# Performance work log

Measured on AMD Instinct MI355X. Metric: run time of the kernel, lower is better.

Reference implementation:

```python
import jax, jax.numpy as jnp
import numpy as np

D_IN = 2048
D_OUT = 2048
NUM_HEADS = 16
NUM_KV_GROUPS = 4
GROUP_SIZE = NUM_HEADS // NUM_KV_GROUPS  # 4
HEAD_DIM = D_OUT // NUM_HEADS            # 128


def setup_inputs() -> dict:
    key = jax.random.key(0)
    ks = jax.random.split(key, 6)
    b, n = 2, 2048
    x = jax.random.normal(ks[0], (b, n, D_IN), dtype=jnp.float32)
    # weights stored as [in, out] so that x @ W matches torch's x @ weight.T
    Wq = jax.random.normal(ks[1], (D_IN, D_OUT), dtype=jnp.float32) * (1.0 / np.sqrt(D_IN))
    Wk = jax.random.normal(ks[2], (D_IN, NUM_KV_GROUPS * HEAD_DIM), dtype=jnp.float32) * (1.0 / np.sqrt(D_IN))
    Wv = jax.random.normal(ks[3], (D_IN, NUM_KV_GROUPS * HEAD_DIM), dtype=jnp.float32) * (1.0 / np.sqrt(D_IN))
    Wo = jax.random.normal(ks[4], (D_OUT, D_OUT), dtype=jnp.float32) * (1.0 / np.sqrt(D_OUT))
    bo = jax.random.normal(ks[5], (D_OUT,), dtype=jnp.float32) * 0.01
    return {"x": x, "Wq": Wq, "Wk": Wk, "Wv": Wv, "Wo": Wo, "bo": bo}


def reference(x, Wq, Wk, Wv, Wo, bo):
    b, n, _ = x.shape
    # projections
    q = (x @ Wq).reshape(b, n, NUM_KV_GROUPS, GROUP_SIZE, HEAD_DIM)  # [b,n,g,s,d]
    k = (x @ Wk).reshape(b, n, NUM_KV_GROUPS, HEAD_DIM)              # [b,n,g,d]
    v = (x @ Wv).reshape(b, n, NUM_KV_GROUPS, HEAD_DIM)
    scale = 1.0 / np.sqrt(HEAD_DIM).astype(np.float32)
    # scores: each group of GROUP_SIZE query heads shares one K/V head
    scores = jnp.einsum('bqgsd,bkgd->bgsqk', q, k) * scale  # [b,g,s,n,n]
    causal = jnp.arange(n)[:, None] < jnp.arange(n)[None, :]  # True above diagonal
    scores = jnp.where(causal, -jnp.inf, scores)
    attn = jax.nn.softmax(scores, axis=-1)
    # dropout omitted for determinism (eval-mode equivalent)
    ctx = jnp.einsum('bgsqk,bkgd->bqgsd', attn, v)  # [b,n,g,s,d]
    ctx = ctx.reshape(b, n, D_OUT)
    return ctx @ Wo + bo
```

## Files before the change

### kernel.cpp

```cpp
#include <hip/hip_runtime.h>
#include <hip/hip_bf16.h>

typedef short bf16x8 __attribute__((ext_vector_type(8)));
typedef float f32x4 __attribute__((ext_vector_type(4)));
typedef float f32x16 __attribute__((ext_vector_type(16)));
typedef unsigned int u32x4 __attribute__((ext_vector_type(4)));

#define MFMA16(a, b, c) __builtin_amdgcn_mfma_f32_16x16x32_bf16((a), (b), (c), 0, 0, 0)
#define MFMA32(a, b, c) __builtin_amdgcn_mfma_f32_32x32x16_bf16((a), (b), (c), 0, 0, 0)

static __device__ __forceinline__ unsigned short f2bf(float f) {
  union { float f; unsigned u; } v;
  v.f = f;
  unsigned r = (v.u + 0x7FFFu + ((v.u >> 16) & 1u)) >> 16;
  return (unsigned short)r;
}

static __device__ __forceinline__ unsigned pk2(float a, float b) {
  unsigned ua = __float_as_uint(a) + 0x8000u;
  unsigned ub = __float_as_uint(b) + 0x8000u;
  return (ua >> 16) | (ub & 0xFFFF0000u);
}

static __device__ __forceinline__ void gload16(const void* g, void* l) {
  __builtin_amdgcn_global_load_lds(
      (const __attribute__((address_space(1))) unsigned int*)g,
      (__attribute__((address_space(3))) unsigned int*)l, 16, 0, 0);
}

__global__ __launch_bounds__(256) void prep_all2(
    const float* __restrict__ x, unsigned short* __restrict__ Xb,
    const float* __restrict__ Wq, const float* __restrict__ Wk,
    const float* __restrict__ Wv, const float* __restrict__ Wo,
    unsigned short* __restrict__ WqT, unsigned short* __restrict__ WkT,
    unsigned short* __restrict__ WvT, unsigned short* __restrict__ WoT) {
  int id = blockIdx.x;
  if (id >= 10240) {
    const int n4 = (4096 * 2048) / 4;
    const int stride = 2048 * 256;
    for (int i = (id - 10240) * 256 + threadIdx.x; i < n4; i += stride) {
      float4 v = reinterpret_cast<const float4*>(x)[i];
      ushort4 o;
      o.x = f2bf(v.x); o.y = f2bf(v.y); o.z = f2bf(v.z); o.w = f2bf(v.w);
      reinterpret_cast<ushort4*>(Xb)[i] = o;
    }
    return;
  }
  __shared__ float tile[32][33];
  const float* src; unsigned short* dst; int R, C, bx, by;
  if (id < 4096)      { src = Wq; dst = WqT; R = 2048; C = 2048; bx = id & 63; by = id >> 6; }
  else if (id < 5120) { id -= 4096; src = Wk; dst = WkT; R = 2048; C = 512; bx = id & 15; by = id >> 4; }
  else if (id < 6144) { id -= 5120; src = Wv; dst = WvT; R = 2048; C = 512; bx = id & 15; by = id >> 4; }
  else                { id -= 6144; src = Wo; dst = WoT; R = 2048; C = 2048; bx = id & 63; by = id >> 6; }
  int tx = threadIdx.x & 31;
  int ty = threadIdx.x >> 5;
  int r0 = by * 32, c0 = bx * 32;
#pragma unroll
  for (int i = 0; i < 32; i += 8)
    tile[ty + i][tx] = src[(size_t)(r0 + ty + i) * C + (c0 + tx)];
  __syncthreads();
#pragma unroll
  for (int i = 0; i < 32; i += 8)
    dst[(size_t)(c0 + ty + i) * R + (r0 + tx)] = f2bf(tile[tx][ty + i]);
}

template <int EPI>
static __device__ __forceinline__ void g8p_core(
    const unsigned short* __restrict__ A, const unsigned short* __restrict__ B,
    unsigned short* __restrict__ Cb, unsigned short* __restrict__ Cb2,
    float* __restrict__ Cf, const float* __restrict__ bias,
    int N, int K, int bid, unsigned short* Al, unsigned short* Bl) {
  const int tid = threadIdx.x;
  const int wave = tid >> 6, lane = tid & 63;
  const int l15 = lane & 15, l4 = lane >> 4;
  const int tilesN = N >> 7;
  const int bm = bid / tilesN, bn = bid % tilesN;
  const int row0 = bm << 8, col0 = bn << 7;
  const int wr = (wave >> 1) << 6;
  const int wc = (wave & 1) << 6;

  const unsigned short* sA[4];
  const unsigned short* sB[2];
#pragma unroll
  for (int i = 0; i < 4; ++i) {
    int q = i * 512 + wave * 64 + lane;
    int r = q >> 3, c = (q & 7) ^ (r & 7);
    sA[i] = A + (size_t)(row0 + r) * K + c * 8;
  }
#pragma unroll
  for (int i = 0; i < 2; ++i) {
    int q = i * 512 + wave * 64 + lane;
    int r = q >> 3, c = (q & 7) ^ (r & 7);
    sB[i] = B + (size_t)(col0 + r) * K + c * 8;
  }

#define STG_H1(t_, bi)                                                      \
  { const size_t ko = (size_t)(t_) * 64;                                    \
    gload16(sA[0] + ko, &Al[(bi)*16384 + (0 * 512 + wave * 64) * 8]);       \
    gload16(sA[1] + ko, &Al[(bi)*16384 + (1 * 512 + wave * 64) * 8]);       \
    gload16(sB[0] + ko, &Bl[(bi)*8192 + (0 * 512 + wave * 64) * 8]); }
#define STG_H2(t_, bi)                                                      \
  { const size_t ko = (size_t)(t_) * 64;                                    \
    gload16(sA[2] + ko, &Al[(bi)*16384 + (2 * 512 + wave * 64) * 8]);       \
    gload16(sA[3] + ko, &Al[(bi)*16384 + (3 * 512 + wave * 64) * 8]);       \
    gload16(sB[1] + ko, &Bl[(bi)*8192 + (1 * 512 + wave * 64) * 8]); }

  const int sw = l15 & 7;
  const int c0 = (l4 ^ sw) << 4;
  const int c1 = ((4 + l4) ^ sw) << 4;
  const int rbA = (wr + l15) << 7;
  const int rbB = (wc + l15) << 7;

  f32x4 acc[4][4] = {};
  const int NT = K >> 6;

  STG_H1(0, 0); STG_H2(0, 0);
  STG_H1(1, 1); STG_H2(1, 1);

  int cur = 0;
  for (int t = 0; t < NT; ++t) {
    int sb = cur + 2; if (sb >= 3) sb -= 3;
    if (t + 1 < NT) { asm volatile("s_waitcnt vmcnt(6)" ::: "memory"); }
    else            { asm volatile("s_waitcnt vmcnt(0)" ::: "memory"); }
    __builtin_amdgcn_s_barrier();
    asm volatile("" ::: "memory");
    const char* Ab = (const char*)&Al[cur * 16384];
    const char* Bb = (const char*)&Bl[cur * 8192];
    bf16x8 b0[4], b1[4], aA[2][2], aB[2][2];
#pragma unroll
    for (int n = 0; n < 4; ++n) {
      b0[n] = *(const bf16x8*)(Bb + rbB + n * 2048 + c0);
      b1[n] = *(const bf16x8*)(Bb + rbB + n * 2048 + c1);
    }
#pragma unroll
    for (int m = 0; m < 2; ++m) {
      aA[m][0] = *(const bf16x8*)(Ab + rbA + m * 2048 + c0);
      aA[m][1] = *(const bf16x8*)(Ab + rbA + m * 2048 + c1);
    }
    if (t + 2 < NT) STG_H1(t + 2, sb);
    asm volatile("" ::: "memory");
    __builtin_amdgcn_s_barrier();
    asm volatile("" ::: "memory");
    __builtin_amdgcn_s_setprio(1);
#pragma unroll
    for (int m = 0; m < 2; ++m)
#pragma unroll
      for (int n = 0; n < 4; ++n) {
        acc[m][n] = MFMA16(aA[m][0], b0[n], acc[m][n]);
        acc[m][n] = MFMA16(aA[m][1], b1[n], acc[m][n]);
      }
    __builtin_amdgcn_s_setprio(0);
#pragma unroll
    for (int m = 0; m < 2; ++m) {
      aB[m][0] = *(const bf16x8*)(Ab + rbA + (m + 2) * 2048 + c0);
      aB[m][1] = *(const bf16x8*)(Ab + rbA + (m + 2) * 2048 + c1);
    }
    if (t + 2 < NT) STG_H2(t + 2, sb);
    asm volatile("" ::: "memory");
    __builtin_amdgcn_s_barrier();
    asm volatile("" ::: "memory");
    __builtin_amdgcn_s_setprio(1);
#pragma unroll
    for (int m = 0; m < 2; ++m)
#pragma unroll
      for (int n = 0; n < 4; ++n) {
        acc[m + 2][n] = MFMA16(aB[m][0], b0[n], acc[m + 2][n]);
        acc[m + 2][n] = MFMA16(aB[m][1], b1[n], acc[m + 2][n]);
      }
    __builtin_amdgcn_s_setprio(0);
    cur += 1; if (cur >= 3) cur = 0;
  }
#undef STG_H1
#undef STG_H2

#pragma unroll
  for (int m = 0; m < 4; ++m) {
#pragma unroll
    for (int n = 0; n < 4; ++n) {
      int row = row0 + wr + m * 16 + l4 * 4;
      int col = col0 + wc + n * 16 + l15;
#pragma unroll
      for (int r = 0; r < 4; ++r) {
        if (EPI == 0) {
          Cb[(size_t)(row + r) * N + col] = f2bf(acc[m][n][r]);
        } else if (EPI == 1) {
          Cf[(size_t)(row + r) * N + col] = acc[m][n][r] + bias[col];
        } else {
          if (col < 2048) Cb[(size_t)(row + r) * 2048 + col] = f2bf(acc[m][n][r]);
          else            Cb2[(size_t)(row + r) * 512 + col - 2048] = f2bf(acc[m][n][r]);
        }
      }
    }
  }
}

__global__ __launch_bounds__(512, 2) void gemm8p_o(
    const unsigned short* __restrict__ A, const unsigned short* __restrict__ B,
    float* __restrict__ Cf, const float* __restrict__ bias, int N, int K) {
  __shared__ unsigned short Al[3 * 256 * 64];
  __shared__ unsigned short Bl[3 * 128 * 64];
  g8p_core<1>(A, B, nullptr, nullptr, Cf, bias, N, K, blockIdx.x, Al, Bl);
}

__global__ __launch_bounds__(512, 2) void gemm_fused3(
    const unsigned short* __restrict__ Xb, const unsigned short* __restrict__ Bqk,
    unsigned short* __restrict__ Qb, unsigned short* __restrict__ Kb,
    const unsigned short* __restrict__ WvT, unsigned short* __restrict__ VTb) {
  __shared__ unsigned short Al[3 * 256 * 64];
  __shared__ unsigned short Bl[3 * 128 * 64];
  if (blockIdx.x < 320)
    g8p_core<2>(Xb, Bqk, Qb, Kb, nullptr, nullptr, 2560, 2048, blockIdx.x, Al, Bl);
  else
    g8p_core<0>(WvT, Xb, VTb, nullptr, nullptr, nullptr, 4096, 2048, blockIdx.x - 320, Al, Bl);
}

__global__ __launch_bounds__(256, 2) void flash_gqa7c(
    const unsigned short* __restrict__ Qb, const unsigned short* __restrict__ Kb,
    const unsigned short* __restrict__ VT, unsigned short* __restrict__ Ctx) {
  __shared__ unsigned short Sm[32768];

  const int tid = threadIdx.x;
  const int wave = tid >> 6, lane = tid & 63;
  const int l31 = lane & 31, hi = lane >> 5;
  const int i = blockIdx.x >> 3;
  const int bg = blockIdx.x & 7;
  const int qt = (i < 32) ? i : (95 - i);
  const int b = bg >> 2, g = bg & 3;
  const int h = (g << 2) | wave;
  const int q0 = qt << 5;
  const int T = (qt >> 1) + 1;

  bf16x8 qf[8];
  {
    const unsigned short* qp =
        Qb + (size_t)(b * 2048 + q0 + l31) * 2048 + h * 128 + hi * 8;
#pragma unroll
    for (int ds = 0; ds < 8; ++ds) qf[ds] = *(const bf16x8*)(qp + ds * 16);
  }

  const int cK = tid & 15, rK = tid >> 4;
  const unsigned short* kS0 = Kb + (size_t)(b * 2048 + rK +  0) * 512 + g * 128 + (cK ^ ((rK +  0) & 7)) * 8;
  const unsigned short* kS1 = Kb + (size_t)(b * 2048 + rK + 16) * 512 + g * 128 + (cK ^ ((rK + 16) & 7)) * 8;
  const unsigned short* kS2 = Kb + (size_t)(b * 2048 + rK + 32) * 512 + g * 128 + (cK ^ ((rK + 32) & 7)) * 8;
  const unsigned short* kS3 = Kb + (size_t)(b * 2048 + rK + 48) * 512 + g * 128 + (cK ^ ((rK + 48) & 7)) * 8;
  const int cV = tid & 7, rV = tid >> 3;
  const unsigned short* vS0 = VT + (size_t)(g * 128 + rV +  0) * 4096 + b * 2048 + (cV ^ ((rV +  0) & 7)) * 8;
  const unsigned short* vS1 = VT + (size_t)(g * 128 + rV + 32) * 4096 + b * 2048 + (cV ^ ((rV + 32) & 7)) * 8;
  const unsigned short* vS2 = VT + (size_t)(g * 128 + rV + 64) * 4096 + b * 2048 + (cV ^ ((rV + 64) & 7)) * 8;
  const unsigned short* vS3 = VT + (size_t)(g * 128 + rV + 96) * 4096 + b * 2048 + (cV ^ ((rV + 96) & 7)) * 8;

#define STAGE7(t_, bi)                                          \
  {                                                             \
    unsigned short* kb_ = Sm + (bi)*8192;                       \
    unsigned short* vb_ = Sm + 16384 + (bi)*8192;               \
    const size_t ko_ = (size_t)(t_) * 64 * 512;                 \
    const size_t vo_ = (size_t)(t_) * 64;                       \
    gload16(kS0 + ko_, kb_ + 0 * 2048 + wave * 512);            \
    gload16(kS1 + ko_, kb_ + 1 * 2048 + wave * 512);            \
    gload16(kS2 + ko_, kb_ + 2 * 2048 + wave * 512);            \
    gload16(kS3 + ko_, kb_ + 3 * 2048 + wave * 512);            \
    gload16(vS0 + vo_, vb_ + 0 * 2048 + wave * 512);            \
    gload16(vS1 + vo_, vb_ + 1 * 2048 + wave * 512);            \
    gload16(vS2 + vo_, vb_ + 2 * 2048 + wave * 512);            \
    gload16(vS3 + vo_, vb_ + 3 * 2048 + wave * 512);            \
  }

  const float s2 = 0.12751744f;
  float m_r = -1e30f, l_r = 0.f;
  f32x16 o0 = {}, o1 = {}, o2 = {}, o3 = {};

  STAGE7(0, 0);
  __syncthreads();

  for (int t = 0; t < T; ++t) {
    const int buf = t & 1;
    if (t + 1 < T) STAGE7(t + 1, buf ^ 1);
    const char* Kl = (const char*)Sm + buf * 16384;
    const char* Vl = (const char*)Sm + 32768 + buf * 16384;
    const int kv = t << 6;
    f32x16 st0 = {}, st1 = {};
    __builtin_amdgcn_s_setprio(1);
#pragma unroll
    for (int ds = 0; ds < 8; ++ds) {
      const int c = ds * 32 + hi * 16;
      const int by0 = (l31 * 256 + c) ^ ((l31 & 7) << 4);
      const int by1 = ((32 + l31) * 256 + c) ^ ((l31 & 7) << 4);
      bf16x8 kf0 = *(const bf16x8*)(Kl + by0);
      bf16x8 kf1 = *(const bf16x8*)(Kl + by1);
      st0 = MFMA32(kf0, qf[ds], st0);
      st1 = MFMA32(kf1, qf[ds], st1);
    }
    __builtin_amdgcn_s_setprio(0);
    const int q_abs = q0 + l31;
    if (kv + 64 > q0) {
#pragma unroll
      for (int rr = 0; rr < 16; ++rr) {
        const int koff = (rr & 3) + 8 * (rr >> 2) + 4 * hi;
        if (kv + koff > q_abs) st0[rr] = -1e30f;
        if (kv + 32 + koff > q_abs) st1[rr] = -1e30f;
      }
    }
    float pm = st0[0];
#pragma unroll
    for (int rr = 1; rr < 16; ++rr) pm = fmaxf(pm, st0[rr]);
#pragma unroll
    for (int rr = 0; rr < 16; ++rr) pm = fmaxf(pm, st1[rr]);
    pm = fmaxf(pm, __shfl_xor(pm, 32));
    if (!__all(pm - m_r <= 90.0f)) {
      const float mn = fmaxf(m_r, pm);
      const float osc = exp2f((m_r - mn) * s2);
      m_r = mn;
      l_r *= osc;
#pragma unroll
      for (int rr = 0; rr < 16; ++rr) {
        o0[rr] *= osc; o1[rr] *= osc; o2[rr] *= osc; o3[rr] *= osc;
      }
    }
    const float cfold = -m_r * s2;
    float ps = 0.f;
#pragma unroll
    for (int rr = 0; rr < 16; ++rr) { st0[rr] = exp2f(fmaf(st0[rr], s2, cfold)); ps += st0[rr]; }
#pragma unroll
    for (int rr = 0; rr < 16; ++rr) { st1[rr] = exp2f(fmaf(st1[rr], s2, cfold)); ps += st1[rr]; }
    ps += __shfl_xor(ps, 32);
    l_r += ps;
    unsigned w0[8], w1[8];
#pragma unroll
    for (int rp = 0; rp < 8; ++rp) {
      w0[rp] = pk2(st0[2 * rp], st0[2 * rp + 1]);
      w1[rp] = pk2(st1[2 * rp], st1[2 * rp + 1]);
    }
    __builtin_amdgcn_s_setprio(1);
#define PV_KS(ks, W)                                                          \
    {                                                                         \
      const int k4 = ((ks) & 1) * 4;                                          \
      unsigned a0 = W[k4], a1 = W[k4 + 1], b0 = W[k4 + 2], b1 = W[k4 + 3];    \
      unsigned q0_ = hi ? a0 : b0, q1_ = hi ? a1 : b1;                        \
      unsigned e0 = (unsigned)__shfl_xor((int)q0_, 32);                       \
      unsigned e1 = (unsigned)__shfl_xor((int)q1_, 32);                       \
      union { u32x4 u; bf16x8 v; } pk;                                        \
      pk.u[0] = hi ? e0 : a0; pk.u[1] = hi ? e1 : a1;                         \
      pk.u[2] = hi ? b0 : e0; pk.u[3] = hi ? b1 : e1;                         \
      const int cb = (ks)*32 + hi * 16;                                       \
      { const int row = l31;      const int by = (row * 128 + cb) ^ ((row & 7) << 4); \
        bf16x8 vf = *(const bf16x8*)(Vl + by); o0 = MFMA32(vf, pk.v, o0); }   \
      { const int row = 32 + l31; const int by = (row * 128 + cb) ^ ((row & 7) << 4); \
        bf16x8 vf = *(const bf16x8*)(Vl + by); o1 = MFMA32(vf, pk.v, o1); }   \
      { const int row = 64 + l31; const int by = (row * 128 + cb) ^ ((row & 7) << 4); \
        bf16x8 vf = *(const bf16x8*)(Vl + by); o2 = MFMA32(vf, pk.v, o2); }   \
      { const int row = 96 + l31; const int by = (row * 128 + cb) ^ ((row & 7) << 4); \
        bf16x8 vf = *(const bf16x8*)(Vl + by); o3 = MFMA32(vf, pk.v, o3); }   \
    }
    PV_KS(0, w0) PV_KS(1, w0) PV_KS(2, w1) PV_KS(3, w1)
#undef PV_KS
    __builtin_amdgcn_s_setprio(0);
    __syncthreads();
  }
#undef STAGE7

  const float inv = 1.f / l_r;
  unsigned short* cp = Ctx + (size_t)(b * 2048 + q0 + l31) * 2048 + h * 128;
#pragma unroll
  for (int a = 0; a < 4; ++a) {
    ushort4 p0, p1, p2, p3;
    p0.x = f2bf(o0[4 * a + 0] * inv); p0.y = f2bf(o0[4 * a + 1] * inv);
    p0.z = f2bf(o0[4 * a + 2] * inv); p0.w = f2bf(o0[4 * a + 3] * inv);
    p1.x = f2bf(o1[4 * a + 0] * inv); p1.y = f2bf(o1[4 * a + 1] * inv);
    p1.z = f2bf(o1[4 * a + 2] * inv); p1.w = f2bf(o1[4 * a + 3] * inv);
    p2.x = f2bf(o2[4 * a + 0] * inv); p2.y = f2bf(o2[4 * a + 1] * inv);
    p2.z = f2bf(o2[4 * a + 2] * inv); p2.w = f2bf(o2[4 * a + 3] * inv);
    p3.x = f2bf(o3[4 * a + 0] * inv); p3.y = f2bf(o3[4 * a + 1] * inv);
    p3.z = f2bf(o3[4 * a + 2] * inv); p3.w = f2bf(o3[4 * a + 3] * inv);
    const int cc = 8 * a + 4 * hi;
    *(ushort4*)(cp + 0 * 32 + cc) = p0;
    *(ushort4*)(cp + 1 * 32 + cc) = p1;
    *(ushort4*)(cp + 2 * 32 + cc) = p2;
    *(ushort4*)(cp + 3 * 32 + cc) = p3;
  }
}

extern "C" void kernel_launch(void* const* d_in, const int* in_sizes, int n_in,
                              void* d_out, int out_size, void* d_ws, size_t ws_size,
                              hipStream_t stream) {
  (void)in_sizes; (void)n_in; (void)out_size; (void)ws_size;
  const float* x  = (const float*)d_in[0];
  const float* Wq = (const float*)d_in[1];
  const float* Wk = (const float*)d_in[2];
  const float* Wv = (const float*)d_in[3];
  const float* Wo = (const float*)d_in[4];
  const float* bo = (const float*)d_in[5];
  float* out = (float*)d_out;

  unsigned short* Xb  = (unsigned short*)d_ws;
  unsigned short* WqT = Xb  + (size_t)4096 * 2048;
  unsigned short* WkT = WqT + (size_t)2048 * 2048;
  unsigned short* WvT = WkT + (size_t)512 * 2048;
  unsigned short* WoT = WvT + (size_t)512 * 2048;
  unsigned short* Qb  = WoT + (size_t)2048 * 2048;
  unsigned short* Kb  = Qb  + (size_t)4096 * 2048;
  unsigned short* VTb = Kb  + (size_t)4096 * 512;
  unsigned short* Ctx = VTb + (size_t)512 * 4096;

  prep_all2<<<12288, 256, 0, stream>>>(x, Xb, Wq, Wk, Wv, Wo, WqT, WkT, WvT, WoT);

  gemm_fused3<<<dim3(384), 512, 0, stream>>>(Xb, WqT, Qb, Kb, WvT, VTb);

  flash_gqa7c<<<dim3(512), 256, 0, stream>>>(Qb, Kb, VTb, Ctx);

  gemm8p_o<<<dim3(256), 512, 0, stream>>>(Ctx, WoT, out, bo, 2048, 2048);
}
```

Measured before the change: 192.8 us.

## Load V fragments directly from global memory and remap GEMM block indices

The flash attention kernel no longer stages V tiles through shared memory. Each lane reads its V^T fragment straight from global memory inside the PV loop, which halves LDS use per block and could allow more resident blocks. The cost is global-load latency sitting directly in the MFMA dependency chain. Separately, the GEMM kernels remap blockIdx so that consecutively launched blocks are spread across XCDs in a strided order, aiming at better L2 locality.

New measurement: 240.8 us. 1.25x slower.

```diff
diff --git a/kernel.cpp b/kernel.cpp
--- a/kernel.cpp
+++ b/kernel.cpp
@@ -199,7 +199,8 @@
     float* __restrict__ Cf, const float* __restrict__ bias, int N, int K) {
   __shared__ unsigned short Al[3 * 256 * 64];
   __shared__ unsigned short Bl[3 * 128 * 64];
-  g8p_core<1>(A, B, nullptr, nullptr, Cf, bias, N, K, blockIdx.x, Al, Bl);
+  int bid = (blockIdx.x & 7) * 32 + (blockIdx.x >> 3);
+  g8p_core<1>(A, B, nullptr, nullptr, Cf, bias, N, K, bid, Al, Bl);
 }
 
 __global__ __launch_bounds__(512, 2) void gemm_fused3(
@@ -208,16 +209,20 @@
     const unsigned short* __restrict__ WvT, unsigned short* __restrict__ VTb) {
   __shared__ unsigned short Al[3 * 256 * 64];
   __shared__ unsigned short Bl[3 * 128 * 64];
-  if (blockIdx.x < 320)
-    g8p_core<2>(Xb, Bqk, Qb, Kb, nullptr, nullptr, 2560, 2048, blockIdx.x, Al, Bl);
-  else
-    g8p_core<0>(WvT, Xb, VTb, nullptr, nullptr, nullptr, 4096, 2048, blockIdx.x - 320, Al, Bl);
-}
-
-__global__ __launch_bounds__(256, 2) void flash_gqa7c(
+  if (blockIdx.x < 320) {
+    int bid = (blockIdx.x & 7) * 40 + (blockIdx.x >> 3);
+    g8p_core<2>(Xb, Bqk, Qb, Kb, nullptr, nullptr, 2560, 2048, bid, Al, Bl);
+  } else {
+    int lb = blockIdx.x - 320;
+    int bid = (lb & 7) * 8 + (lb >> 3);
+    g8p_core<0>(WvT, Xb, VTb, nullptr, nullptr, nullptr, 4096, 2048, bid, Al, Bl);
+  }
+}
+
+__global__ __launch_bounds__(256, 2) void flash_gqa7d(
     const unsigned short* __restrict__ Qb, const unsigned short* __restrict__ Kb,
     const unsigned short* __restrict__ VT, unsigned short* __restrict__ Ctx) {
-  __shared__ unsigned short Sm[32768];
+  __shared__ unsigned short Sm[16384];
 
   const int tid = threadIdx.x;
   const int wave = tid >> 6, lane = tid & 63;
@@ -243,26 +248,20 @@
   const unsigned short* kS1 = Kb + (size_t)(b * 2048 + rK + 16) * 512 + g * 128 + (cK ^ ((rK + 16) & 7)) * 8;
   const unsigned short* kS2 = Kb + (size_t)(b * 2048 + rK + 32) * 512 + g * 128 + (cK ^ ((rK + 32) & 7)) * 8;
   const unsigned short* kS3 = Kb + (size_t)(b * 2048 + rK + 48) * 512 + g * 128 + (cK ^ ((rK + 48) & 7)) * 8;
-  const int cV = tid & 7, rV = tid >> 3;
-  const unsigned short* vS0 = VT + (size_t)(g * 128 + rV +  0) * 4096 + b * 2048 + (cV ^ ((rV +  0) & 7)) * 8;
-  const unsigned short* vS1 = VT + (size_t)(g * 128 + rV + 32) * 4096 + b * 2048 + (cV ^ ((rV + 32) & 7)) * 8;
-  const unsigned short* vS2 = VT + (size_t)(g * 128 + rV + 64) * 4096 + b * 2048 + (cV ^ ((rV + 64) & 7)) * 8;
-  const unsigned short* vS3 = VT + (size_t)(g * 128 + rV + 96) * 4096 + b * 2048 + (cV ^ ((rV + 96) & 7)) * 8;
+
+  const unsigned short* vG0 = VT + (size_t)(g * 128 +  0 + l31) * 4096 + b * 2048 + hi * 8;
+  const unsigned short* vG1 = VT + (size_t)(g * 128 + 32 + l31) * 4096 + b * 2048 + hi * 8;
+  const unsigned short* vG2 = VT + (size_t)(g * 128 + 64 + l31) * 4096 + b * 2048 + hi * 8;
+  const unsigned short* vG3 = VT + (size_t)(g * 128 + 96 + l31) * 4096 + b * 2048 + hi * 8;
 
 #define STAGE7(t_, bi)                                          \
   {                                                             \
     unsigned short* kb_ = Sm + (bi)*8192;                       \
-    unsigned short* vb_ = Sm + 16384 + (bi)*8192;               \
     const size_t ko_ = (size_t)(t_) * 64 * 512;                 \
-    const size_t vo_ = (size_t)(t_) * 64;                       \
     gload16(kS0 + ko_, kb_ + 0 * 2048 + wave * 512);            \
     gload16(kS1 + ko_, kb_ + 1 * 2048 + wave * 512);            \
     gload16(kS2 + ko_, kb_ + 2 * 2048 + wave * 512);            \
     gload16(kS3 + ko_, kb_ + 3 * 2048 + wave * 512);            \
-    gload16(vS0 + vo_, vb_ + 0 * 2048 + wave * 512);            \
-    gload16(vS1 + vo_, vb_ + 1 * 2048 + wave * 512);            \
-    gload16(vS2 + vo_, vb_ + 2 * 2048 + wave * 512);            \
-    gload16(vS3 + vo_, vb_ + 3 * 2048 + wave * 512);            \
   }
 
   const float s2 = 0.12751744f;
@@ -276,8 +275,11 @@
     const int buf = t & 1;
     if (t + 1 < T) STAGE7(t + 1, buf ^ 1);
     const char* Kl = (const char*)Sm + buf * 16384;
-    const char* Vl = (const char*)Sm + 32768 + buf * 16384;
     const int kv = t << 6;
+    const unsigned short* vP0 = vG0 + kv;
+    const unsigned short* vP1 = vG1 + kv;
+    const unsigned short* vP2 = vG2 + kv;
+    const unsigned short* vP3 = vG3 + kv;
     f32x16 st0 = {}, st1 = {};
     __builtin_amdgcn_s_setprio(1);
 #pragma unroll
@@ -341,15 +343,10 @@
       union { u32x4 u; bf16x8 v; } pk;                                        \
       pk.u[0] = hi ? e0 : a0; pk.u[1] = hi ? e1 : a1;                         \
       pk.u[2] = hi ? b0 : e0; pk.u[3] = hi ? b1 : e1;                         \
-      const int cb = (ks)*32 + hi * 16;                                       \
-      { const int row = l31;      const int by = (row * 128 + cb) ^ ((row & 7) << 4); \
-        bf16x8 vf = *(const bf16x8*)(Vl + by); o0 = MFMA32(vf, pk.v, o0); }   \
-      { const int row = 32 + l31; const int by = (row * 128 + cb) ^ ((row & 7) << 4); \
-        bf16x8 vf = *(const bf16x8*)(Vl + by); o1 = MFMA32(vf, pk.v, o1); }   \
-      { const int row = 64 + l31; const int by = (row * 128 + cb) ^ ((row & 7) << 4); \
-        bf16x8 vf = *(const bf16x8*)(Vl + by); o2 = MFMA32(vf, pk.v, o2); }   \
-      { const int row = 96 + l31; const int by = (row * 128 + cb) ^ ((row & 7) << 4); \
-        bf16x8 vf = *(const bf16x8*)(Vl + by); o3 = MFMA32(vf, pk.v, o3); }   \
+      { bf16x8 vf = *(const bf16x8*)(vP0 + (ks)*16); o0 = MFMA32(vf, pk.v, o0); } \
+      { bf16x8 vf = *(const bf16x8*)(vP1 + (ks)*16); o1 = MFMA32(vf, pk.v, o1); } \
+      { bf16x8 vf = *(const bf16x8*)(vP2 + (ks)*16); o2 = MFMA32(vf, pk.v, o2); } \
+      { bf16x8 vf = *(const bf16x8*)(vP3 + (ks)*16); o3 = MFMA32(vf, pk.v, o3); } \
     }
     PV_KS(0, w0) PV_KS(1, w0) PV_KS(2, w1) PV_KS(3, w1)
 #undef PV_KS
@@ -405,7 +402,7 @@
 
   gemm_fused3<<<dim3(384), 512, 0, stream>>>(Xb, WqT, Qb, Kb, WvT, VTb);
 
-  flash_gqa7c<<<dim3(512), 256, 0, stream>>>(Qb, Kb, VTb, Ctx);
+  flash_gqa7d<<<dim3(512), 256, 0, stream>>>(Qb, Kb, VTb, Ctx);
 
   gemm8p_o<<<dim3(256), 512, 0, stream>>>(Ctx, WoT, out, bo, 2048, 2048);
 }
```
